# Kernel tuning notes

Measured on AMD Instinct MI355X. Metric: run time of the kernel, lower is better.

Reference implementation:

```python
import jax, jax.numpy as jnp
import numpy as np

B, N, FDIM = 2, 512, 1024
HEADS, DH = 4, 256          # out_per_head = 1024 // 4
AH = 256                    # attn_hidden
HID, OUT, NCLS = 512, 128, 10
RATIO, TEMP = 0.8, 0.5


def setup_inputs() -> dict:
    key = jax.random.key(0)
    ks = jax.random.split(key, 16)
    g = lambda i, shape, s: (jax.random.normal(ks[i], shape, dtype=jnp.float32) * s)
    return {
        "x": g(0, (B, N, FDIM), 1.0),
        # GATLayer
        "Wg": g(1, (FDIM, FDIM), 0.02),          # linear weight [out,in], no bias
        "attn": g(2, (HEADS, 2 * DH), 0.05),
        # CausalAttNetV1 edge_mlp: Linear(2F,AH) -> ReLU -> Linear(AH,1)
        "W1": g(3, (AH, 2 * FDIM), 0.02),
        "b1": jnp.zeros((AH,), jnp.float32),
        "w2": g(4, (AH,), 0.05),
        "b2": jnp.zeros((), jnp.float32),
        # GCN
        "gc1_w": g(5, (HID, FDIM), 0.03), "gc1_b": jnp.zeros((HID,), jnp.float32),
        "bn1_g": jnp.ones((HID,), jnp.float32), "bn1_b": jnp.zeros((HID,), jnp.float32),
        "gc2_w": g(6, (OUT, HID), 0.04), "gc2_b": jnp.zeros((OUT,), jnp.float32),
        "bn2_g": jnp.ones((OUT,), jnp.float32), "bn2_b": jnp.zeros((OUT,), jnp.float32),
        # classifier
        "cls_w": g(7, (NCLS, OUT), 0.1), "cls_b": jnp.zeros((NCLS,), jnp.float32),
    }


def _batchnorm(h, gamma, beta):
    # BatchNorm1d in training mode over the flattened (B*N, F) dim, biased var.
    m = h.mean(axis=(0, 1))
    v = jnp.mean((h - m) ** 2, axis=(0, 1))
    return (h - m) * jax.lax.rsqrt(v + 1e-5) * gamma + beta


def _forward(x, Wg, attn, W1, b1, w2, b2,
             gc1_w, gc1_b, bn1_g, bn1_b, gc2_w, gc2_b, bn2_g, bn2_b,
             cls_w, cls_b):
    # ---- GATLayer (adj=None) ----
    hp = jnp.einsum('bnf,of->bno', x, Wg)                     # [B,N,1024]
    hp = hp.reshape(B, N, HEADS, DH).transpose(0, 2, 1, 3)     # [B,H,N,DH]
    a_i, a_j = attn[:, :DH], attn[:, DH:]
    s_i = jnp.einsum('bhnd,hd->bhn', hp, a_i)                  # source score
    s_j = jnp.einsum('bhnd,hd->bhn', hp, a_j)                  # target score
    e = s_i[:, :, :, None] + s_j[:, :, None, :]                # [B,H,N,N]
    e = jnp.where(e >= 0, e, 0.2 * e)                          # LeakyReLU(0.2)
    alpha = jax.nn.softmax(e, axis=-1)
    hn = jnp.einsum('bhij,bhjd->bhid', alpha, hp)
    node_feats = hn.transpose(0, 2, 1, 3).reshape(B, N, HEADS * DH)  # [B,N,1024]

    # ---- CausalAttNetV1 (split cat-linear into row/col halves) ----
    W1i, W1j = W1[:, :FDIM], W1[:, FDIM:]
    pi = jnp.einsum('bnf,af->bna', node_feats, W1i)            # [B,N,AH]
    pj = jnp.einsum('bnf,af->bna', node_feats, W1j)
    hid = jax.nn.relu(pi[:, :, None, :] + pj[:, None, :, :] + b1)  # [B,N,N,AH]
    edge_scores = jnp.einsum('bija,a->bij', hid, w2) + b2      # [B,N,N]
    flat = edge_scores.reshape(B, N * N)
    soft_mask = jax.nn.softmax(flat / TEMP, axis=1)
    k = int(RATIO * N * N)
    thr = jnp.sort(soft_mask, axis=1)[:, -k]                   # k-th largest value
    cm = jnp.where(soft_mask >= thr[:, None], soft_mask, 0.0)
    cm = cm / (cm.sum(axis=1, keepdims=True) + 1e-12)
    causal_adj = cm.reshape(B, N, N)

    # ---- GCN (return_embeddings=True) ----
    h = jnp.einsum('bij,bjf->bif', causal_adj, node_feats)
    h = jnp.einsum('bif,of->bio', h, gc1_w) + gc1_b
    h = jax.nn.relu(_batchnorm(h, bn1_g, bn1_b))
    h = jnp.einsum('bij,bjf->bif', causal_adj, h)
    h = jnp.einsum('bif,of->bio', h, gc2_w) + gc2_b
    h = jax.nn.relu(_batchnorm(h, bn2_g, bn2_b))

    # ---- classify (mode='pred') ----
    feat_causal = h.mean(axis=1)                               # [B,128]
    return jnp.einsum('bf,cf->bc', feat_causal, cls_w) + cls_b # [B,NCLS]


def reference(x, Wg, attn, W1, b1, w2, b2,
              gc1_w, gc1_b, bn1_g, bn1_b, gc2_w, gc2_b, bn2_g, bn2_b,
              cls_w, cls_b):
    return _forward(x, Wg, attn, W1, b1, w2, b2,
                    gc1_w, gc1_b, bn1_g, bn1_b, gc2_w, gc2_b, bn2_g, bn2_b,
                    cls_w, cls_b)
```

## Files before the change

kernel.cpp:

```cpp
#include <hip/hip_runtime.h>
#include <hip/hip_bf16.h>


__global__ __launch_bounds__(256) void gemm64_nt(
    const float* __restrict__ A, const float* __restrict__ Bm, float* __restrict__ C,
    int K, int lda, int ldb, int ldc, const float* __restrict__ bias,
    const float* __restrict__ Bm2, float* __restrict__ C2, const float* __restrict__ bias2,
    int ksplit, long pstride)
{
    if (ksplit > 1){
        int z = blockIdx.z;
        int kz = z % ksplit;
        if (z / ksplit){ Bm = Bm2; C = C2; bias = bias2; }
        A += (size_t)kz * K; Bm += (size_t)kz * K;
        C += (long)kz * pstride;
        if (kz) bias = nullptr;
    } else if (blockIdx.z){
        Bm = Bm2; C = C2; bias = bias2;
    }
    __shared__ float As[64][64], Bs[64][64];
    int t = threadIdx.x;
    int m0 = blockIdx.y*64, n0 = blockIdx.x*64;
    int w = t>>6, lane = t&63;
    int mi = lane>>3, ni = lane&7;
    int kc = w*16;
    const float* Ar = A + (size_t)(m0+lane)*lda + kc;
    const float* Br = Bm + (size_t)(n0+lane)*ldb + kc;
    float4 pa[4], pb[4];
    #pragma unroll
    for (int j=0;j<4;++j){ pa[j]=*(const float4*)(Ar+j*4); pb[j]=*(const float4*)(Br+j*4); }
    float acc[8][8] = {};
    for (int k0=0; k0<K; k0+=64){
        #pragma unroll
        for (int j=0;j<4;++j){
            As[kc+j*4+0][lane]=pa[j].x; As[kc+j*4+1][lane]=pa[j].y;
            As[kc+j*4+2][lane]=pa[j].z; As[kc+j*4+3][lane]=pa[j].w;
            Bs[kc+j*4+0][lane]=pb[j].x; Bs[kc+j*4+1][lane]=pb[j].y;
            Bs[kc+j*4+2][lane]=pb[j].z; Bs[kc+j*4+3][lane]=pb[j].w;
        }
        if (k0+64 < K){
            #pragma unroll
            for (int j=0;j<4;++j){
                pa[j]=*(const float4*)(Ar+k0+64+j*4);
                pb[j]=*(const float4*)(Br+k0+64+j*4);
            }
        }
        #pragma unroll
        for (int kk=0; kk<16; ++kk){
            float4 a0=*(const float4*)&As[kc+kk][mi*8], a1=*(const float4*)&As[kc+kk][mi*8+4];
            float4 b0=*(const float4*)&Bs[kc+kk][ni*8], b1=*(const float4*)&Bs[kc+kk][ni*8+4];
            float am[8]={a0.x,a0.y,a0.z,a0.w,a1.x,a1.y,a1.z,a1.w};
            float bn[8]={b0.x,b0.y,b0.z,b0.w,b1.x,b1.y,b1.z,b1.w};
            #pragma unroll
            for (int i=0;i<8;++i)
                #pragma unroll
                for (int j2=0;j2<8;++j2) acc[i][j2] += am[i]*bn[j2];
        }
    }
    __syncthreads();
    float* s0 = &As[0][0]; float* s1 = &Bs[0][0];
    if (w>=2){
        float* d = (w==2)? s0 : s1;
        #pragma unroll
        for (int i=0;i<8;++i){
            *(float4*)&d[(mi*8+i)*64+ni*8]   = make_float4(acc[i][0],acc[i][1],acc[i][2],acc[i][3]);
            *(float4*)&d[(mi*8+i)*64+ni*8+4] = make_float4(acc[i][4],acc[i][5],acc[i][6],acc[i][7]);
        }
    }
    __syncthreads();
    if (w<2){
        const float* sv = (w==0)? s0 : s1;
        #pragma unroll
        for (int i=0;i<8;++i){
            float4 v0=*(const float4*)&sv[(mi*8+i)*64+ni*8];
            float4 v1=*(const float4*)&sv[(mi*8+i)*64+ni*8+4];
            acc[i][0]+=v0.x; acc[i][1]+=v0.y; acc[i][2]+=v0.z; acc[i][3]+=v0.w;
            acc[i][4]+=v1.x; acc[i][5]+=v1.y; acc[i][6]+=v1.z; acc[i][7]+=v1.w;
        }
    }
    __syncthreads();
    if (w==1){
        #pragma unroll
        for (int i=0;i<8;++i){
            *(float4*)&s0[(mi*8+i)*64+ni*8]   = make_float4(acc[i][0],acc[i][1],acc[i][2],acc[i][3]);
            *(float4*)&s0[(mi*8+i)*64+ni*8+4] = make_float4(acc[i][4],acc[i][5],acc[i][6],acc[i][7]);
        }
    }
    __syncthreads();
    if (w==0){
        #pragma unroll
        for (int i=0;i<8;++i){
            float4 v0=*(const float4*)&s0[(mi*8+i)*64+ni*8];
            float4 v1=*(const float4*)&s0[(mi*8+i)*64+ni*8+4];
            acc[i][0]+=v0.x; acc[i][1]+=v0.y; acc[i][2]+=v0.z; acc[i][3]+=v0.w;
            acc[i][4]+=v1.x; acc[i][5]+=v1.y; acc[i][6]+=v1.z; acc[i][7]+=v1.w;
        }
        float bb[8];
        #pragma unroll
        for (int j2=0;j2<8;++j2) bb[j2] = bias ? bias[n0+ni*8+j2] : 0.f;
        #pragma unroll
        for (int i=0;i<8;++i){
            *(float4*)&C[(size_t)(m0+mi*8+i)*ldc + n0+ni*8]   =
                make_float4(acc[i][0]+bb[0],acc[i][1]+bb[1],acc[i][2]+bb[2],acc[i][3]+bb[3]);
            *(float4*)&C[(size_t)(m0+mi*8+i)*ldc + n0+ni*8+4] =
                make_float4(acc[i][4]+bb[4],acc[i][5]+bb[5],acc[i][6]+bb[6],acc[i][7]+bb[7]);
        }
    }
}

__global__ __launch_bounds__(256) void gemm64_nn(
    const float* __restrict__ A, const float* __restrict__ Bm, float* __restrict__ C,
    int K, int lda, int ldb, int ldc, long sA, long sB, long sC,
    const float* __restrict__ bsc, const float* __restrict__ bsh, int bhmode,
    int ksplit, long pstride)
{
    if (bhmode){
        int z = blockIdx.z;
        A  += (size_t)z*sA;
        Bm += (size_t)(z>>2)*sB + (size_t)(z&3)*256;
        C  += (size_t)(z>>2)*sC + (size_t)(z&3)*256;
    } else {
        int z = blockIdx.z;
        int bz = z, kz = 0;
        if (ksplit > 1){ bz = z / ksplit; kz = z % ksplit; }
        A  += (long)bz*sA + (size_t)kz*K;
        Bm += (long)bz*sB + (size_t)kz*K*ldb;
        C  += (long)bz*sC + (long)kz*pstride;
    }
    __shared__ float As[64][64], Bs[64][64];
    int t=threadIdx.x, w=t>>6, lane=t&63;
    int m0=blockIdx.y*64, n0=blockIdx.x*64;
    int mi=lane>>3, ni=lane&7;
    int kc=w*16;
    const float* Ar = A + (size_t)(m0+lane)*lda + kc;
    int kr = lane>>4, nc = (lane&15)*4;
    const float* Br = Bm + (size_t)(kc+kr)*ldb + n0 + nc;
    float4 sc4 = make_float4(1,1,1,1), sh4 = make_float4(0,0,0,0);
    if (bsc){ sc4 = *(const float4*)&bsc[n0+nc]; sh4 = *(const float4*)&bsh[n0+nc]; }
    float4 pa[4], pb[4];
    #pragma unroll
    for (int j=0;j<4;++j){
        pa[j]=*(const float4*)(Ar+j*4);
        pb[j]=*(const float4*)(Br + (size_t)(j*4)*ldb);
    }
    float acc[8][8] = {};
    for (int k0=0; k0<K; k0+=64){
        #pragma unroll
        for (int j=0;j<4;++j){
            As[kc+j*4+0][lane]=pa[j].x; As[kc+j*4+1][lane]=pa[j].y;
            As[kc+j*4+2][lane]=pa[j].z; As[kc+j*4+3][lane]=pa[j].w;
            float4 bv = pb[j];
            if (bsc){
                bv.x=fmaxf(bv.x*sc4.x+sh4.x,0.f); bv.y=fmaxf(bv.y*sc4.y+sh4.y,0.f);
                bv.z=fmaxf(bv.z*sc4.z+sh4.z,0.f); bv.w=fmaxf(bv.w*sc4.w+sh4.w,0.f);
            }
            *(float4*)&Bs[kc+kr+j*4][nc] = bv;
        }
        if (k0+64 < K){
            #pragma unroll
            for (int j=0;j<4;++j){
                pa[j]=*(const float4*)(Ar+k0+64+j*4);
                pb[j]=*(const float4*)(Br + (size_t)(k0+64+j*4)*ldb);
            }
        }
        #pragma unroll
        for (int kk=0; kk<16; ++kk){
            float4 a0=*(const float4*)&As[kc+kk][mi*8], a1=*(const float4*)&As[kc+kk][mi*8+4];
            float4 b0=*(const float4*)&Bs[kc+kk][ni*8], b1=*(const float4*)&Bs[kc+kk][ni*8+4];
            float am[8]={a0.x,a0.y,a0.z,a0.w,a1.x,a1.y,a1.z,a1.w};
            float bn[8]={b0.x,b0.y,b0.z,b0.w,b1.x,b1.y,b1.z,b1.w};
            #pragma unroll
            for (int i=0;i<8;++i)
                #pragma unroll
                for (int j2=0;j2<8;++j2) acc[i][j2] += am[i]*bn[j2];
        }
    }
    __syncthreads();
    float* s0 = &As[0][0]; float* s1 = &Bs[0][0];
    if (w>=2){
        float* d = (w==2)? s0 : s1;
        #pragma unroll
        for (int i=0;i<8;++i){
            *(float4*)&d[(mi*8+i)*64+ni*8]   = make_float4(acc[i][0],acc[i][1],acc[i][2],acc[i][3]);
            *(float4*)&d[(mi*8+i)*64+ni*8+4] = make_float4(acc[i][4],acc[i][5],acc[i][6],acc[i][7]);
        }
    }
    __syncthreads();
    if (w<2){
        const float* sv = (w==0)? s0 : s1;
        #pragma unroll
        for (int i=0;i<8;++i){
            float4 v0=*(const float4*)&sv[(mi*8+i)*64+ni*8];
            float4 v1=*(const float4*)&sv[(mi*8+i)*64+ni*8+4];
            acc[i][0]+=v0.x; acc[i][1]+=v0.y; acc[i][2]+=v0.z; acc[i][3]+=v0.w;
            acc[i][4]+=v1.x; acc[i][5]+=v1.y; acc[i][6]+=v1.z; acc[i][7]+=v1.w;
        }
    }
    __syncthreads();
    if (w==1){
        #pragma unroll
        for (int i=0;i<8;++i){
            *(float4*)&s0[(mi*8+i)*64+ni*8]   = make_float4(acc[i][0],acc[i][1],acc[i][2],acc[i][3]);
            *(float4*)&s0[(mi*8+i)*64+ni*8+4] = make_float4(acc[i][4],acc[i][5],acc[i][6],acc[i][7]);
        }
    }
    __syncthreads();
    if (w==0){
        #pragma unroll
        for (int i=0;i<8;++i){
            float4 v0=*(const float4*)&s0[(mi*8+i)*64+ni*8];
            float4 v1=*(const float4*)&s0[(mi*8+i)*64+ni*8+4];
            acc[i][0]+=v0.x; acc[i][1]+=v0.y; acc[i][2]+=v0.z; acc[i][3]+=v0.w;
            acc[i][4]+=v1.x; acc[i][5]+=v1.y; acc[i][6]+=v1.z; acc[i][7]+=v1.w;
        }
        #pragma unroll
        for (int i=0;i<8;++i){
            *(float4*)&C[(size_t)(m0+mi*8+i)*ldc + n0+ni*8]   =
                make_float4(acc[i][0],acc[i][1],acc[i][2],acc[i][3]);
            *(float4*)&C[(size_t)(m0+mi*8+i)*ldc + n0+ni*8+4] =
                make_float4(acc[i][4],acc[i][5],acc[i][6],acc[i][7]);
        }
    }
}

__global__ void foldk(float* __restrict__ dst, const float* __restrict__ src,
                      long pstride, int kparts, int n4){
    int i = blockIdx.x*256 + threadIdx.x;
    if (i < n4){
        float4 s = *(const float4*)&src[(size_t)i*4];
        for (int p=1;p<kparts;++p){
            float4 v = *(const float4*)&src[(long)p*pstride + (size_t)i*4];
            s.x+=v.x; s.y+=v.y; s.z+=v.z; s.w+=v.w;
        }
        *(float4*)&dst[(size_t)i*4] = s;
    }
}

__global__ void transp_v15(const float* __restrict__ PJ, float* __restrict__ pjT){
    __shared__ float T[64][68];
    int b = blockIdx.z;
    int a0 = blockIdx.x*64, n0 = blockIdx.y*64;
    int t = threadIdx.x;
    int c = t&15, r = t>>4;
    for (int rr=r; rr<64; rr+=16){
        float4 v = *(const float4*)&PJ[(size_t)(b*512+n0+rr)*256 + a0 + c*4];
        T[rr][c*4]=v.x; T[rr][c*4+1]=v.y; T[rr][c*4+2]=v.z; T[rr][c*4+3]=v.w;
    }
    __syncthreads();
    for (int rr=r; rr<64; rr+=16){
        float4 o = make_float4(T[c*4][rr], T[c*4+1][rr], T[c*4+2][rr], T[c*4+3][rr]);
        *(float4*)&pjT[(size_t)b*131072 + (size_t)(a0+rr)*512 + n0 + c*4] = o;
    }
}

__global__ void bnp1(const float* __restrict__ src, float* __restrict__ PS,
                     float* __restrict__ PS2, int F){
    int f0 = blockIdx.x*64, r0 = blockIdx.y*64;
    int fi = threadIdx.x & 63, rg = threadIdx.x >> 6;
    float s=0.f, s2=0.f;
    #pragma unroll
    for (int i=0;i<16;++i){
        float v = src[(size_t)(r0+rg+i*4)*F + f0+fi];
        s += v; s2 += v*v;
    }
    __shared__ float ls[4][64], ls2[4][64];
    ls[rg][fi]=s; ls2[rg][fi]=s2; __syncthreads();
    if (rg==0){
        PS [blockIdx.y*F + f0+fi] = ls[0][fi]+ls[1][fi]+ls[2][fi]+ls[3][fi];
        PS2[blockIdx.y*F + f0+fi] = ls2[0][fi]+ls2[1][fi]+ls2[2][fi]+ls2[3][fi];
    }
}

__global__ void bnp2(const float* __restrict__ PS, const float* __restrict__ PS2,
                     const float* __restrict__ g, const float* __restrict__ be,
                     float* __restrict__ scale, float* __restrict__ shift, int F){
    int f = blockIdx.x*64 + threadIdx.x;
    float S=0.f, S2=0.f;
    #pragma unroll
    for (int c=0;c<16;++c){ S += PS[c*F+f]; S2 += PS2[c*F+f]; }
    float m  = S*(1.f/1024.f);
    float var = S2*(1.f/1024.f) - m*m;
    float sc = g[f] * rsqrtf(var + 1e-5f);
    scale[f]=sc; shift[f]=be[f] - m*sc;
}

__global__ void feat_p(const float* __restrict__ h4, const float* __restrict__ sc,
                       const float* __restrict__ sh, float* __restrict__ featp){
    int b = blockIdx.x, chunk = blockIdx.y;
    int t = threadIdx.x;
    float s = sc[t], o = sh[t], acc = 0.f;
    int n0 = chunk*64;
    #pragma unroll
    for (int i=0;i<64;++i){
        float v = h4[(size_t)(b*512+n0+i)*128 + t]*s + o;
        acc += fmaxf(v, 0.f);
    }
    featp[(b*8+chunk)*128 + t] = acc;
}

__global__ void feat_f(const float* __restrict__ featp, float* __restrict__ feat){
    int b = blockIdx.x, t = threadIdx.x;
    float a = 0.f;
    #pragma unroll
    for (int c=0;c<8;++c) a += featp[(b*8+c)*128 + t];
    feat[b*128+t] = a*(1.f/512.f);
}

__global__ void gemm_nn32(const float* __restrict__ A, const float* __restrict__ Bm,
                          float* __restrict__ C, int K, int lda, int ldb, int ldc,
                          long sA, long sB, long sC,
                          const float* __restrict__ bsc, const float* __restrict__ bsh){
    A  += (long)blockIdx.z * sA;
    Bm += (long)blockIdx.z * sB;
    C  += (long)blockIdx.z * sC;
    __shared__ float As[16][32], Bs[16][64];
    int n0 = blockIdx.x*64, m0 = blockIdx.y*32;
    int t = threadIdx.x, tx = t & 15, ty = t >> 4;
    int sr = t >> 3, sk = (t & 7)*2;
    int bk = t >> 4, bn4 = (t & 15)*4;
    float acc[2][4] = {};
    for (int k0=0; k0<K; k0+=16){
        #pragma unroll
        for (int i=0;i<2;++i) As[sk+i][sr] = A[(size_t)(m0+sr)*lda + k0+sk+i];
        float4 bv = *(const float4*)&Bm[(size_t)(k0+bk)*ldb + n0+bn4];
        if (bsc){
            bv.x = fmaxf(bv.x*bsc[n0+bn4+0]+bsh[n0+bn4+0], 0.f);
            bv.y = fmaxf(bv.y*bsc[n0+bn4+1]+bsh[n0+bn4+1], 0.f);
            bv.z = fmaxf(bv.z*bsc[n0+bn4+2]+bsh[n0+bn4+2], 0.f);
            bv.w = fmaxf(bv.w*bsc[n0+bn4+3]+bsh[n0+bn4+3], 0.f);
        }
        *(float4*)&Bs[bk][bn4] = bv;
        __syncthreads();
        #pragma unroll
        for (int k=0;k<16;++k){
            float a0 = As[k][ty*2], a1 = As[k][ty*2+1];
            float4 b = *(const float4*)&Bs[k][tx*4];
            acc[0][0]+=a0*b.x; acc[0][1]+=a0*b.y; acc[0][2]+=a0*b.z; acc[0][3]+=a0*b.w;
            acc[1][0]+=a1*b.x; acc[1][1]+=a1*b.y; acc[1][2]+=a1*b.z; acc[1][3]+=a1*b.w;
        }
        __syncthreads();
    }
    #pragma unroll
    for (int i=0;i<2;++i){
        float4 v = make_float4(acc[i][0],acc[i][1],acc[i][2],acc[i][3]);
        *(float4*)&C[(size_t)(m0+ty*2+i)*ldc + n0+tx*4] = v;
    }
}

__global__ void gemm_nt32(const float* __restrict__ A, const float* __restrict__ Bm,
                          float* __restrict__ C, int K, int lda, int ldb, int ldc,
                          const float* __restrict__ bias){
    __shared__ float As[16][32], Bs[16][64];
    int n0 = blockIdx.x*64, m0 = blockIdx.y*32;
    int t = threadIdx.x, tx = t & 15, ty = t >> 4;
    int sr = t >> 3, sk = (t & 7)*2;
    int bn = t >> 2, bkk = (t & 3)*4;
    float acc[2][4] = {};
    for (int k0=0; k0<K; k0+=16){
        #pragma unroll
        for (int i=0;i<2;++i) As[sk+i][sr] = A[(size_t)(m0+sr)*lda + k0+sk+i];
        float4 wv = *(const float4*)&Bm[(size_t)(n0+bn)*ldb + k0+bkk];
        Bs[bkk+0][bn]=wv.x; Bs[bkk+1][bn]=wv.y; Bs[bkk+2][bn]=wv.z; Bs[bkk+3][bn]=wv.w;
        __syncthreads();
        #pragma unroll
        for (int k=0;k<16;++k){
            float a0 = As[k][ty*2], a1 = As[k][ty*2+1];
            float4 b = *(const float4*)&Bs[k][tx*4];
            acc[0][0]+=a0*b.x; acc[0][1]+=a0*b.y; acc[0][2]+=a0*b.z; acc[0][3]+=a0*b.w;
            acc[1][0]+=a1*b.x; acc[1][1]+=a1*b.y; acc[1][2]+=a1*b.z; acc[1][3]+=a1*b.w;
        }
        __syncthreads();
    }
    float4 bb = bias ? *(const float4*)&bias[n0+tx*4] : make_float4(0,0,0,0);
    #pragma unroll
    for (int i=0;i<2;++i){
        float4 v = make_float4(acc[i][0]+bb.x,acc[i][1]+bb.y,acc[i][2]+bb.z,acc[i][3]+bb.w);
        *(float4*)&C[(size_t)(m0+ty*2+i)*ldc + n0+tx*4] = v;
    }
}

__global__ void gemm_x_v12(const float* __restrict__ X, const float* __restrict__ Wg,
                           float* __restrict__ dst){
    __shared__ float xs[4][1024];
    int m0 = blockIdx.x*4;
    int t = threadIdx.x;
    for (int i=t;i<4096;i+=256){ int r=i>>10, c=i&1023; xs[r][c]=X[(size_t)(m0+r)*1024+c]; }
    __syncthreads();
    const float* w0 = Wg + (size_t)(t*4)*1024;
    float acc[4][4] = {};
    for (int k0=0;k0<1024;k0+=16){
        float4 xv[4][4];
        #pragma unroll
        for (int r=0;r<4;++r)
            #pragma unroll
            for (int c=0;c<4;++c) xv[r][c] = *(const float4*)&xs[r][k0+4*c];
        #pragma unroll
        for (int j=0;j<4;++j){
            const float* wr = w0 + (size_t)j*1024 + k0;
            #pragma unroll
            for (int c=0;c<4;++c){
                float4 w = *(const float4*)(wr + 4*c);
                #pragma unroll
                for (int r=0;r<4;++r)
                    acc[r][j] += xv[r][c].x*w.x + xv[r][c].y*w.y
                               + xv[r][c].z*w.z + xv[r][c].w*w.w;
            }
        }
    }
    int n0 = t*4;
    #pragma unroll
    for (int r=0;r<4;++r){
        float4 v = make_float4(acc[r][0],acc[r][1],acc[r][2],acc[r][3]);
        *(float4*)&dst[(size_t)(m0+r)*1024 + n0] = v;
    }
}

__global__ void attn_v12(const float* __restrict__ hp, const float* __restrict__ attn,
                         float* __restrict__ nf){
    int blk = blockIdx.x;
    int bh = blk >> 6, i0 = (blk & 63)*8;
    int b = bh >> 2, h = bh & 3;
    int t = threadIdx.x;
    __shared__ float ais[256], ajs[256], sjs[512], sis[8], inv[8];
    __shared__ float alpha[8][512];
    __shared__ float red[256];
    ais[t] = attn[h*512 + t];
    ajs[t] = attn[h*512 + 256 + t];
    __syncthreads();
    const float* hpb = hp + (size_t)b*524288 + h*256;
    for (int j=t; j<512; j+=256){
        const float* row = hpb + (size_t)j*1024;
        float s=0.f;
        for (int d=0; d<256; ++d) s += row[d]*ajs[d];
        sjs[j]=s;
    }
    if (t<8){
        const float* row = hpb + (size_t)(i0+t)*1024;
        float s=0.f;
        for (int d=0; d<256; ++d) s += row[d]*ais[d];
        sis[t]=s;
    }
    __syncthreads();
    for (int ii=0; ii<8; ++ii){
        float si = sis[ii];
        float e0 = si + sjs[t], e1 = si + sjs[t+256];
        e0 = (e0>=0.f)? e0 : 0.2f*e0;
        e1 = (e1>=0.f)? e1 : 0.2f*e1;
        float p0 = expf(e0), p1 = expf(e1);
        alpha[ii][t]=p0; alpha[ii][t+256]=p1;
        red[t]=p0+p1; __syncthreads();
        for (int s=128; s>0; s>>=1){ if (t<s) red[t]+=red[t+s]; __syncthreads(); }
        if (t==0) inv[ii] = 1.0f/red[0];
        __syncthreads();
    }
    float acc[8] = {};
    for (int j=0; j<512; ++j){
        float r = hpb[(size_t)j*1024 + t];
        #pragma unroll
        for (int ii=0; ii<8; ++ii) acc[ii] += alpha[ii][j]*r;
    }
    #pragma unroll
    for (int ii=0; ii<8; ++ii)
        nf[(size_t)(b*512+i0+ii)*1024 + h*256 + t] = acc[ii]*inv[ii];
}

__global__ void sij_v14(const float* __restrict__ hp, const float* __restrict__ attn,
                        float* __restrict__ SI, float* __restrict__ SJ){
    int t = threadIdx.x;
    int lane = t & 63, w = t >> 6;
    int h  = lane >> 4;
    int e0 = (lane & 15) * 16;
    const float* ai = attn + h*512 + e0;
    const float* aj = ai + 256;
    float4 wi[4], wj[4];
    #pragma unroll
    for (int q=0;q<4;++q){ wi[q] = *(const float4*)(ai + 4*q); wj[q] = *(const float4*)(aj + 4*q); }
    int row0 = blockIdx.x*16 + w*4;
    for (int r=0;r<4;++r){
        int row = row0 + r;
        const float* hr = hp + (size_t)row*1024 + h*256 + e0;
        float si=0.f, sj=0.f;
        #pragma unroll
        for (int q=0;q<4;++q){
            float4 v = *(const float4*)(hr + 4*q);
            si += v.x*wi[q].x + v.y*wi[q].y + v.z*wi[q].z + v.w*wi[q].w;
            sj += v.x*wj[q].x + v.y*wj[q].y + v.z*wj[q].z + v.w*wj[q].w;
        }
        #pragma unroll
        for (int s=1;s<16;s<<=1){
            si += __shfl_xor(si, s, 64);
            sj += __shfl_xor(sj, s, 64);
        }
        if ((lane & 15)==0){
            int b = row >> 9, n = row & 511;
            SI[(size_t)(b*4+h)*512 + n] = si;
            SJ[(size_t)(b*4+h)*512 + n] = sj;
        }
    }
}

__global__ __launch_bounds__(512) void asm_v17(const float* __restrict__ SI,
                                               const float* __restrict__ SJ,
                                               float* __restrict__ ALP){
    int blk = blockIdx.x;
    int bh = blk >> 5, i0 = (blk & 31)*16;
    int t = threadIdx.x;
    int w = t >> 6, lane = t & 63;
    __shared__ float wsum[8][16];
    __shared__ float inv[16];
    float sj = SJ[(size_t)bh*512 + t];
    const float* sip = SI + (size_t)bh*512 + i0;
    float p[16], part[16];
    #pragma unroll
    for (int ii=0; ii<16; ++ii){
        float e = sip[ii] + sj;
        e = (e>=0.f)? e : 0.2f*e;
        p[ii] = expf(e);
        part[ii] = p[ii];
    }
    #pragma unroll
    for (int s=1;s<64;s<<=1){
        #pragma unroll
        for (int ii=0;ii<16;++ii) part[ii] += __shfl_xor(part[ii], s, 64);
    }
    if (lane==0){
        #pragma unroll
        for (int ii=0;ii<16;++ii) wsum[w][ii] = part[ii];
    }
    __syncthreads();
    if (t<16){
        float s=0.f;
        #pragma unroll
        for (int ww=0;ww<8;++ww) s += wsum[ww][t];
        inv[t] = 1.0f/s;
    }
    __syncthreads();
    float* dst = ALP + (size_t)bh*262144 + (size_t)i0*512 + t;
    #pragma unroll
    for (int ii=0; ii<16; ++ii)
        dst[(size_t)ii*512] = p[ii]*inv[ii];
}

__global__ void pipj_v13(const float* __restrict__ nf, const float* __restrict__ W1,
                         const float* __restrict__ b1, float* __restrict__ pi,
                         float* __restrict__ pjT){
    int half = blockIdx.z >> 5;
    int m0 = (blockIdx.z & 31)*32;
    int a0 = blockIdx.x*64;
    __shared__ float As[16][32], Bs[16][64];
    int t = threadIdx.x, tx = t & 15, ty = t >> 4;
    int sr = t >> 3, sk = (t & 7)*2;
    int bn = t >> 2, bkk = (t & 3)*4;
    const float* Wbase = W1 + (half ? 1024 : 0);
    float acc[2][4] = {};
    for (int k0=0; k0<1024; k0+=16){
        #pragma unroll
        for (int i=0;i<2;++i) As[sk+i][sr] = nf[(size_t)(m0+sr)*1024 + k0+sk+i];
        float4 wv = *(const float4*)&Wbase[(size_t)(a0+bn)*2048 + k0+bkk];
        Bs[bkk+0][bn]=wv.x; Bs[bkk+1][bn]=wv.y; Bs[bkk+2][bn]=wv.z; Bs[bkk+3][bn]=wv.w;
        __syncthreads();
        #pragma unroll
        for (int k=0;k<16;++k){
            float a0v = As[k][ty*2], a1v = As[k][ty*2+1];
            float4 b = *(const float4*)&Bs[k][tx*4];
            acc[0][0]+=a0v*b.x; acc[0][1]+=a0v*b.y; acc[0][2]+=a0v*b.z; acc[0][3]+=a0v*b.w;
            acc[1][0]+=a1v*b.x; acc[1][1]+=a1v*b.y; acc[1][2]+=a1v*b.z; acc[1][3]+=a1v*b.w;
        }
        __syncthreads();
    }
    if (!half){
        float4 bb = *(const float4*)&b1[a0+tx*4];
        #pragma unroll
        for (int i=0;i<2;++i){
            float4 v = make_float4(acc[i][0]+bb.x,acc[i][1]+bb.y,acc[i][2]+bb.z,acc[i][3]+bb.w);
            *(float4*)&pi[(size_t)(m0+ty*2+i)*256 + a0+tx*4] = v;
        }
    } else {
        #pragma unroll
        for (int i=0;i<2;++i){
            int m = m0+ty*2+i;
            size_t base = (size_t)(m>>9)*131072 + (m&511);
            #pragma unroll
            for (int j=0;j<4;++j)
                pjT[base + (size_t)(a0+tx*4+j)*512] = acc[i][j];
        }
    }
}

__global__ void edge_v12(const float* __restrict__ pi, const float* __restrict__ pjT,
                         const float* __restrict__ w2, const float* __restrict__ b2,
                         float* __restrict__ es){
    int blk = blockIdx.x;
    int b = blk >> 7, i0 = (blk & 127)*4;
    int t = threadIdx.x;
    __shared__ float pis[4][256], w2s[256];
    w2s[t] = w2[t];
    #pragma unroll
    for (int r=0;r<4;++r)
        pis[r][t] = pi[(size_t)(b*512+i0+r)*256 + t];
    __syncthreads();
    float a0[4]={0,0,0,0}, a1[4]={0,0,0,0};
    const float* pj = pjT + (size_t)b*131072;
    #pragma unroll 4
    for (int a=0; a<256; ++a){
        float pv0 = pj[(size_t)a*512 + t];
        float pv1 = pj[(size_t)a*512 + t + 256];
        float w  = w2s[a];
        #pragma unroll
        for (int r=0;r<4;++r){
            float p = pis[r][a];
            a0[r] += fmaxf(p+pv0, 0.f)*w;
            a1[r] += fmaxf(p+pv1, 0.f)*w;
        }
    }
    float b2f = b2[0];
    #pragma unroll
    for (int r=0;r<4;++r){
        es[(size_t)(b*512+i0+r)*512 + t]       = a0[r] + b2f;
        es[(size_t)(b*512+i0+r)*512 + t + 256] = a1[r] + b2f;
    }
}

__global__ void k_exp_v14(float* __restrict__ u, float* __restrict__ S,
                          unsigned* __restrict__ hist){
    __shared__ unsigned h[2048];
    __shared__ float red[256];
    int t = threadIdx.x;
    for (int i=t;i<2048;i+=256) h[i]=0;
    __syncthreads();
    int b = blockIdx.x >> 8;
    size_t base = (size_t)b*262144 + (size_t)(blockIdx.x & 255)*1024;
    float acc = 0.f;
    for (int i=t;i<1024;i+=256){
        float v = expf(u[base+i]*2.0f);
        u[base+i]=v; acc+=v;
        atomicAdd(&h[(__float_as_uint(v)>>21)&0x7FFu], 1u);
    }
    red[t]=acc; __syncthreads();
    for (int s=128;s>0;s>>=1){ if(t<s) red[t]+=red[t+s]; __syncthreads(); }
    if (t==0) atomicAdd(&S[b], red[0]);
    for (int i=t;i<2048;i+=256) if (h[i]) atomicAdd(&hist[b*2048+i], h[i]);
}

__global__ void k_hist_v12(const float* __restrict__ u, unsigned* __restrict__ hist,
                           const unsigned* __restrict__ pfx, int cmpShift, int shift,
                           unsigned mask, int nbins){
    __shared__ unsigned h[2048];
    for (int i=threadIdx.x;i<nbins;i+=256) h[i]=0;
    __syncthreads();
    int b = blockIdx.x>>7;
    size_t base = (size_t)b*262144 + (size_t)(blockIdx.x&127)*2048;
    unsigned p = pfx ? pfx[b] : 0u;
    for (int i=threadIdx.x;i<2048;i+=256){
        unsigned bits = __float_as_uint(u[base+i]);
        if (!pfx || (bits>>cmpShift)==p) atomicAdd(&h[(bits>>shift)&mask],1u);
    }
    __syncthreads();
    for (int i=threadIdx.x;i<nbins;i+=256) if (h[i]) atomicAdd(&hist[b*nbins+i], h[i]);
}

__global__ void k_scan_v11(const unsigned* __restrict__ hist, int nbins,
                           unsigned* __restrict__ pfx, unsigned* __restrict__ rank,
                           int passBits, int first, float* __restrict__ thrOut){
    __shared__ unsigned part[2][256];
    int batch = threadIdx.x>>8, lane = threadIdx.x&255;
    int chunk = nbins/256;
    const unsigned* hb = hist + batch*nbins;
    unsigned s=0;
    for (int i=0;i<chunk;++i) s += hb[lane*chunk+i];
    part[batch][lane]=s;
    __syncthreads();
    if (lane==0){
        unsigned r = first ? 52429u : rank[batch];
        unsigned cum=0; int c=0;
        for (;c<256;++c){ unsigned pc=part[batch][c]; if (cum+pc>r) break; cum+=pc; }
        if (c==256) c=255;
        int bin=c*chunk;
        for (int i=0;i<chunk;++i){ unsigned cnt=hb[c*chunk+i]; if (cum+cnt>r){ bin=c*chunk+i; break;} cum+=cnt; }
        rank[batch]=r-cum;
        unsigned np = ((first?0u:pfx[batch])<<passBits) | (unsigned)bin;
        pfx[batch]=np;
        if (thrOut) thrOut[batch]=__uint_as_float(np);
    }
}

__global__ void k_csum_v12(const float* __restrict__ u, const float* __restrict__ THR,
                           float* __restrict__ CS, unsigned* __restrict__ KC){
    int b = blockIdx.x>>7;
    size_t base = (size_t)b*262144 + (size_t)(blockIdx.x&127)*2048;
    float th = THR[b];
    float cs=0.f; unsigned kc=0;
    for (int i=threadIdx.x;i<2048;i+=256){ float v=u[base+i]; if (v>=th){ cs+=v; kc++; } }
    __shared__ float rf[256]; __shared__ unsigned ru[256];
    rf[threadIdx.x]=cs; ru[threadIdx.x]=kc; __syncthreads();
    for (int s=128;s>0;s>>=1){ if(threadIdx.x<s){ rf[threadIdx.x]+=rf[threadIdx.x+s]; ru[threadIdx.x]+=ru[threadIdx.x+s]; } __syncthreads(); }
    if (threadIdx.x==0){ atomicAdd(&CS[b], rf[0]); atomicAdd(&KC[b], ru[0]); }
}

__global__ void k_fin_v11(const float* __restrict__ S, const float* __restrict__ CS,
                          const unsigned* __restrict__ KC, float* __restrict__ THR,
                          float* __restrict__ DINV){
    int t = threadIdx.x;
    if (t < 2){
        float ks = CS[t]; float th = THR[t];
        if (KC[t] < 209715u){ th = 0.f; ks = S[t]; }
        THR[t]=th;
        DINV[t]=1.0f/(ks + 1e-12f*S[t]);
    }
}

__global__ void adj_v10(float* __restrict__ u, const float* __restrict__ thrU,
                        const float* __restrict__ dinv){
    int idx = blockIdx.x*256 + threadIdx.x;
    int b = idx >> 18;
    float v = u[idx];
    u[idx] = (v >= thrU[b]) ? v*dinv[b] : 0.0f;
}

__global__ void bnstats_v10(const float* __restrict__ src, const float* __restrict__ g,
                            const float* __restrict__ be, float* __restrict__ scale,
                            float* __restrict__ shift, int F){
    int f0 = blockIdx.x*64;
    int fi = threadIdx.x & 63, rg = threadIdx.x >> 6;
    float s=0.f, s2=0.f;
    for (int r=rg; r<1024; r+=4){ float v = src[(size_t)r*F + f0+fi]; s+=v; s2+=v*v; }
    __shared__ float ls[4][64], ls2[4][64];
    ls[rg][fi]=s; ls2[rg][fi]=s2; __syncthreads();
    if (rg==0){
        float Sv = ls[0][fi]+ls[1][fi]+ls[2][fi]+ls[3][fi];
        float S2 = ls2[0][fi]+ls2[1][fi]+ls2[2][fi]+ls2[3][fi];
        float m  = Sv*(1.f/1024.f);
        float var = S2*(1.f/1024.f) - m*m;
        float sc = g[f0+fi] * rsqrtf(var + 1e-5f);
        scale[f0+fi]=sc;
        shift[f0+fi]=be[f0+fi] - m*sc;
    }
}

__global__ void feat_v10(const float* __restrict__ h4, const float* __restrict__ sc,
                         const float* __restrict__ sh, float* __restrict__ feat){
    int b = blockIdx.x, t = threadIdx.x;
    float s = sc[t], o = sh[t], acc = 0.f;
    for (int n=0; n<512; ++n){
        float v = h4[(size_t)(b*512+n)*128 + t]*s + o;
        acc += fmaxf(v, 0.f);
    }
    feat[b*128+t] = acc*(1.f/512.f);
}

__global__ void k_exp_v13(float* __restrict__ u, float* __restrict__ S){
    int b = blockIdx.x >> 8;
    size_t base = (size_t)b*262144 + (size_t)(blockIdx.x & 255)*1024;
    int t = threadIdx.x;
    float acc = 0.f;
    for (int i=t;i<1024;i+=256){ float v = expf(u[base+i]*2.0f); u[base+i]=v; acc+=v; }
    __shared__ float red[256];
    red[t]=acc; __syncthreads();
    for (int s=128;s>0;s>>=1){ if(t<s) red[t]+=red[t+s]; __syncthreads(); }
    if (t==0) atomicAdd(&S[b], red[0]);
}

__global__ void cls_v10(const float* __restrict__ feat, const float* __restrict__ cls_w,
                        const float* __restrict__ cls_b, float* __restrict__ out){
    int t = threadIdx.x;
    if (t < 20){
        int b = t/10, c = t%10;
        float acc = cls_b[c];
        for (int o=0; o<128; ++o)
            acc += feat[b*128+o]*cls_w[c*128+o];
        out[t] = acc;
    }
}

extern "C" void kernel_launch(void* const* d_in, const int* in_sizes, int n_in,
                              void* d_out, int out_size, void* d_ws, size_t ws_size,
                              hipStream_t stream){
    (void)in_sizes; (void)n_in; (void)out_size;
    const float* x     = (const float*)d_in[0];
    const float* Wg    = (const float*)d_in[1];
    const float* attn  = (const float*)d_in[2];
    const float* W1    = (const float*)d_in[3];
    const float* b1    = (const float*)d_in[4];
    const float* w2    = (const float*)d_in[5];
    const float* b2    = (const float*)d_in[6];
    const float* gc1_w = (const float*)d_in[7];
    const float* gc1_b = (const float*)d_in[8];
    const float* bn1_g = (const float*)d_in[9];
    const float* bn1_b = (const float*)d_in[10];
    const float* gc2_w = (const float*)d_in[11];
    const float* gc2_b = (const float*)d_in[12];
    const float* bn2_g = (const float*)d_in[13];
    const float* bn2_b = (const float*)d_in[14];
    const float* cls_w = (const float*)d_in[15];
    const float* cls_b = (const float*)d_in[16];
    float* out = (float*)d_out;

    float *HP, *NF, *U, *PI, *PJT, *H1, *H2, *H3, *H4;
    float *STAT, *BN1S, *BN1H, *BN2S, *BN2H, *FEAT;
    float *SIbuf = nullptr, *SJbuf = nullptr, *PJ = nullptr, *ALP = nullptr;
    float *PSb = nullptr, *PS2b = nullptr, *FEATP = nullptr;
    int wsPath = (ws_size >= (size_t)22*1024*1024);

    if (wsPath){
        float* W = (float*)d_ws;
        HP  = W + 0;        NF  = W + 1048576;  H1 = W + 2097152;
        PI  = W + 3145728;  PJT = W + 3407872;  U  = W + 3670016;
        H2  = W + 4194304;  H3  = W + 4718592;  H4 = W + 5242880;
        BN1S= W + 5374208;  BN1H= W + 5374720;
        BN2S= W + 5375232;  BN2H= W + 5375360;  FEAT = W + 5375488;
        STAT= W + 5400000;
        SIbuf = W + 5500000; SJbuf = W + 5504096;
        PJ  = H2;
        ALP = PI;
        PSb = W + 5420000; PS2b = W + 5430000; FEATP = W + 5440000;
    } else {
        HP  = (float*)x;
        NF  = (float*)Wg;
        PI  = (float*)x;
        PJT = (float*)x + 262144;
        U   = (float*)W1;
        H1  = (float*)x;
        H2  = (float*)Wg;
        H3  = (float*)gc1_w;
        H4  = (float*)x;
        STAT= (float*)x;
        float* A = (float*)attn;
        BN1S = A+8;    BN1H = A+520;
        BN2S = A+1032; BN2H = A+1160;  FEAT = A+1288;
    }
    float*    S    = STAT+2;
    float*    CS   = STAT+4;
    unsigned* KC   = (unsigned*)(STAT+6);
    unsigned* PFX  = (unsigned*)(STAT+8);
    unsigned* RANK = (unsigned*)(STAT+10);
    float*    THR  = STAT+12;
    float*    DINV = STAT+14;
    unsigned* H0   = (unsigned*)(STAT+16);
    unsigned* Hh1  = (unsigned*)(STAT+16+4096);
    unsigned* Hh2  = (unsigned*)(STAT+16+8192);

    if (wsPath){
        gemm64_nt<<<dim3(16,16,2),256,0,stream>>>(x, Wg, HP, 512, 1024, 1024, 1024,
                                                  nullptr, nullptr, nullptr, nullptr,
                                                  2, (long)(H1-HP));
        foldk<<<1024,256,0,stream>>>(HP, HP, (long)(H1-HP), 2, 262144);
        sij_v14 <<<64,256,0,stream>>>(HP, attn, SIbuf, SJbuf);
        asm_v17 <<<256,512,0,stream>>>(SIbuf, SJbuf, ALP);
        gemm64_nn<<<dim3(4,8,8),256,0,stream>>>(ALP, HP, NF, 512, 512, 1024, 1024,
                                                262144, 524288, 524288, nullptr, nullptr,
                                                1, 1, 0);
        gemm64_nt<<<dim3(4,16,4),256,0,stream>>>(NF, W1, PI, 512, 1024, 2048, 256,
                                                 b1, W1+1024, PJ, nullptr,
                                                 2, 262144);
        foldk<<<256,256,0,stream>>>(PI, PI, 262144, 2, 65536);
        foldk<<<256,256,0,stream>>>(PJ, PJ, 262144, 2, 65536);
        transp_v15<<<dim3(4,8,2),256,0,stream>>>(PJ, PJT);
    } else {
        gemm_x_v12<<<256,256,0,stream>>>(x, Wg, HP);
        attn_v12  <<<512,256,0,stream>>>(HP, attn, NF);
        pipj_v13  <<<dim3(4,1,64),256,0,stream>>>(NF, W1, b1, PI, PJT);
    }
    edge_v12  <<<256,256,0,stream>>>(PI, PJT, w2, b2, U);
    hipMemsetAsync(STAT, 0, 10256*sizeof(float), stream);
    k_exp_v14 <<<512,256,0,stream>>>(U, S, H0);
    k_scan_v11<<<1,512,0,stream>>>(H0, 2048, PFX, RANK, 11, 1, nullptr);
    k_hist_v12<<<256,256,0,stream>>>(U, Hh1, PFX, 21, 10, 0x7FFu, 2048);
    k_scan_v11<<<1,512,0,stream>>>(Hh1, 2048, PFX, RANK, 11, 0, nullptr);
    k_hist_v12<<<256,256,0,stream>>>(U, Hh2, PFX, 10, 0, 0x3FFu, 1024);
    k_scan_v11<<<1,512,0,stream>>>(Hh2, 1024, PFX, RANK, 10, 0, THR);
    k_csum_v12<<<256,256,0,stream>>>(U, THR, CS, KC);
    k_fin_v11 <<<1,64,0,stream>>>(S, CS, KC, THR, DINV);
    adj_v10   <<<2048,256,0,stream>>>(U, THR, DINV);

    if (wsPath){
        gemm64_nn<<<dim3(16,8,4),256,0,stream>>>(U, NF, H1, 256, 512, 1024, 1024,
                                                 262144, 524288, 524288, nullptr, nullptr,
                                                 0, 2, (long)(HP-H1));
        foldk<<<1024,256,0,stream>>>(H1, H1, (long)(HP-H1), 2, 262144);
        gemm64_nt<<<dim3(8,16,2),256,0,stream>>>(H1, gc1_w, H2, 512, 1024, 1024, 512,
                                                 gc1_b, nullptr, nullptr, nullptr,
                                                 2, (long)(NF-H2));
        foldk<<<512,256,0,stream>>>(H2, H2, (long)(NF-H2), 2, 131072);
        bnp1<<<dim3(8,16),256,0,stream>>>(H2, PSb, PS2b, 512);
        bnp2<<<8,64,0,stream>>>(PSb, PS2b, bn1_g, bn1_b, BN1S, BN1H, 512);
        gemm64_nn<<<dim3(8,8,4),256,0,stream>>>(U, H2, H3, 256, 512, 512, 512,
                                                262144, 262144, 262144, BN1S, BN1H,
                                                0, 2, (long)(HP-H3));
        foldk<<<512,256,0,stream>>>(H3, H3, (long)(HP-H3), 2, 131072);
        gemm64_nt<<<dim3(2,16,4),256,0,stream>>>(H3, gc2_w, HP, 128, 512, 512, 128,
                                                 gc2_b, nullptr, nullptr, nullptr,
                                                 4, 131072);
        foldk<<<128,256,0,stream>>>(H4, HP, 131072, 4, 32768);
        bnp1<<<dim3(2,16),256,0,stream>>>(H4, PSb, PS2b, 128);
        bnp2<<<2,64,0,stream>>>(PSb, PS2b, bn2_g, bn2_b, BN2S, BN2H, 128);
        feat_p<<<dim3(2,8),128,0,stream>>>(H4, BN2S, BN2H, FEATP);
        feat_f<<<2,128,0,stream>>>(FEATP, FEAT);
    } else {
        gemm_nn32 <<<dim3(16,16,2),256,0,stream>>>(U, NF, H1, 512, 512, 1024, 1024,
                                                   262144, 524288, 524288, nullptr, nullptr);
        gemm_nt32 <<<dim3(8,32),256,0,stream>>>(H1, gc1_w, H2, 1024, 1024, 1024, 512, gc1_b);
        bnstats_v10<<<8,256,0,stream>>>(H2, bn1_g, bn1_b, BN1S, BN1H, 512);
        gemm_nn32 <<<dim3(8,16,2),256,0,stream>>>(U, H2, H3, 512, 512, 512, 512,
                                                  262144, 262144, 262144, BN1S, BN1H);
        gemm_nt32 <<<dim3(2,32),256,0,stream>>>(H3, gc2_w, H4, 512, 512, 512, 128, gc2_b);
        bnstats_v10<<<2,256,0,stream>>>(H4, bn2_g, bn2_b, BN2S, BN2H, 128);
        feat_v10  <<<2,128,0,stream>>>(H4, BN2S, BN2H, FEAT);
    }
    cls_v10   <<<1,64,0,stream>>>(FEAT, cls_w, cls_b, out);
}
```

Before: 364.3 us.

## Split-K the attention aggregation GEMM and retile the edge-score kernel

Result: slower. 372.5 us (+2.2%).

```diff
diff --git a/kernel.cpp b/kernel.cpp
--- a/kernel.cpp
+++ b/kernel.cpp
@@ -116,9 +116,11 @@
 {
     if (bhmode){
         int z = blockIdx.z;
-        A  += (size_t)z*sA;
-        Bm += (size_t)(z>>2)*sB + (size_t)(z&3)*256;
-        C  += (size_t)(z>>2)*sC + (size_t)(z&3)*256;
+        int kz = 0;
+        if (ksplit > 1){ kz = z % ksplit; z /= ksplit; }
+        A  += (size_t)z*sA + (size_t)kz*K;
+        Bm += (size_t)(z>>2)*sB + (size_t)(z&3)*256 + (size_t)kz*K*ldb;
+        C  += (size_t)(z>>2)*sC + (size_t)(z&3)*256 + (long)kz*pstride;
     } else {
         int z = blockIdx.z;
         int bz = z, kz = 0;
@@ -587,38 +589,34 @@
     }
 }
 
-__global__ void edge_v12(const float* __restrict__ pi, const float* __restrict__ pjT,
+__global__ void edge_v13(const float* __restrict__ pi, const float* __restrict__ pjT,
                          const float* __restrict__ w2, const float* __restrict__ b2,
                          float* __restrict__ es){
     int blk = blockIdx.x;
-    int b = blk >> 7, i0 = (blk & 127)*4;
-    int t = threadIdx.x;
-    __shared__ float pis[4][256], w2s[256];
+    int b = blk >> 7;
+    int rem = blk & 127;
+    int i0 = (rem >> 1)*8, jh = rem & 1;
+    int t = threadIdx.x;
+    __shared__ float pis[8][256], w2s[256];
     w2s[t] = w2[t];
     #pragma unroll
-    for (int r=0;r<4;++r)
+    for (int r=0;r<8;++r)
         pis[r][t] = pi[(size_t)(b*512+i0+r)*256 + t];
     __syncthreads();
-    float a0[4]={0,0,0,0}, a1[4]={0,0,0,0};
-    const float* pj = pjT + (size_t)b*131072;
+    float acc[8]={0,0,0,0,0,0,0,0};
+    const float* pj = pjT + (size_t)b*131072 + jh*256;
     #pragma unroll 4
     for (int a=0; a<256; ++a){
-        float pv0 = pj[(size_t)a*512 + t];
-        float pv1 = pj[(size_t)a*512 + t + 256];
+        float pv = pj[(size_t)a*512 + t];
         float w  = w2s[a];
         #pragma unroll
-        for (int r=0;r<4;++r){
-            float p = pis[r][a];
-            a0[r] += fmaxf(p+pv0, 0.f)*w;
-            a1[r] += fmaxf(p+pv1, 0.f)*w;
-        }
+        for (int r=0;r<8;++r)
+            acc[r] += fmaxf(pis[r][a]+pv, 0.f)*w;
     }
     float b2f = b2[0];
     #pragma unroll
-    for (int r=0;r<4;++r){
-        es[(size_t)(b*512+i0+r)*512 + t]       = a0[r] + b2f;
-        es[(size_t)(b*512+i0+r)*512 + t + 256] = a1[r] + b2f;
-    }
+    for (int r=0;r<8;++r)
+        es[(size_t)(b*512+i0+r)*512 + jh*256 + t] = acc[r] + b2f;
 }
 
 __global__ void k_exp_v14(float* __restrict__ u, float* __restrict__ S,
@@ -758,6 +756,35 @@
     red[t]=acc; __syncthreads();
     for (int s=128;s>0;s>>=1){ if(t<s) red[t]+=red[t+s]; __syncthreads(); }
     if (t==0) atomicAdd(&S[b], red[0]);
+}
+
+__global__ void edge_v10(const float* __restrict__ pi, const float* __restrict__ pjT,
+                         const float* __restrict__ w2, const float* __restrict__ b2,
+                         float* __restrict__ es){
+    int blk = blockIdx.x;
+    int b = blk >> 8, i0 = (blk & 255)*2;
+    int t = threadIdx.x;
+    __shared__ float pis[2][256], w2s[256];
+    w2s[t] = w2[t];
+    pis[0][t] = pi[(size_t)(b*512+i0)*256 + t];
+    pis[1][t] = pi[(size_t)(b*512+i0+1)*256 + t];
+    __syncthreads();
+    float a00=0,a01=0,a10=0,a11=0;
+    const float* pj = pjT + (size_t)b*131072;
+    for (int a=0; a<256; ++a){
+        float pv0 = pj[(size_t)a*512 + t];
+        float pv1 = pj[(size_t)a*512 + t + 256];
+        float w  = w2s[a];
+        a00 += fmaxf(pis[0][a]+pv0, 0.f)*w;
+        a01 += fmaxf(pis[0][a]+pv1, 0.f)*w;
+        a10 += fmaxf(pis[1][a]+pv0, 0.f)*w;
+        a11 += fmaxf(pis[1][a]+pv1, 0.f)*w;
+    }
+    float b2f = b2[0];
+    es[(size_t)(b*512+i0+0)*512 + t]       = a00 + b2f;
+    es[(size_t)(b*512+i0+0)*512 + t + 256] = a01 + b2f;
+    es[(size_t)(b*512+i0+1)*512 + t]       = a10 + b2f;
+    es[(size_t)(b*512+i0+1)*512 + t + 256] = a11 + b2f;
 }
 
 __global__ void cls_v10(const float* __restrict__ feat, const float* __restrict__ cls_w,
@@ -846,9 +873,10 @@
         foldk<<<1024,256,0,stream>>>(HP, HP, (long)(H1-HP), 2, 262144);
         sij_v14 <<<64,256,0,stream>>>(HP, attn, SIbuf, SJbuf);
         asm_v17 <<<256,512,0,stream>>>(SIbuf, SJbuf, ALP);
-        gemm64_nn<<<dim3(4,8,8),256,0,stream>>>(ALP, HP, NF, 512, 512, 1024, 1024,
-                                                262144, 524288, 524288, nullptr, nullptr,
-                                                1, 1, 0);
+        gemm64_nn<<<dim3(4,8,16),256,0,stream>>>(ALP, HP, NF, 256, 512, 1024, 1024,
+                                                 262144, 524288, 524288, nullptr, nullptr,
+                                                 1, 2, (long)(H1-NF));
+        foldk<<<1024,256,0,stream>>>(NF, NF, (long)(H1-NF), 2, 262144);
         gemm64_nt<<<dim3(4,16,4),256,0,stream>>>(NF, W1, PI, 512, 1024, 2048, 256,
                                                  b1, W1+1024, PJ, nullptr,
                                                  2, 262144);
@@ -860,7 +888,10 @@
         attn_v12  <<<512,256,0,stream>>>(HP, attn, NF);
         pipj_v13  <<<dim3(4,1,64),256,0,stream>>>(NF, W1, b1, PI, PJT);
     }
-    edge_v12  <<<256,256,0,stream>>>(PI, PJT, w2, b2, U);
+    if (wsPath)
+        edge_v13 <<<256,256,0,stream>>>(PI, PJT, w2, b2, U);
+    else
+        edge_v10 <<<512,256,0,stream>>>(PI, PJT, w2, b2, U);
     hipMemsetAsync(STAT, 0, 10256*sizeof(float), stream);
     k_exp_v14 <<<512,256,0,stream>>>(U, S, H0);
     k_scan_v11<<<1,512,0,stream>>>(H0, 2048, PFX, RANK, 11, 1, nullptr);
```
